# Kernel tuning notes

Hardware: AMD Instinct MI355X
Metric: run time of the kernel (lower is better)

Reference implementation:

```python
import jax, jax.numpy as jnp
import numpy as np

N = 100_000      # nodes
E = 1_600_000    # edges (avg degree 16)
D = 64           # dim_node
H = 64           # dim_hidden
L = 4            # model_layer
G = 512          # num graphs
BN_EPS = 1e-5


def setup_inputs() -> dict:
    key = jax.random.key(0)
    ks = jax.random.split(key, 16)
    x = jax.random.normal(ks[0], (N, D), dtype=jnp.float32)
    edge_index = jax.random.randint(ks[1], (2, E), 0, N, dtype=jnp.int64)
    batch = jnp.sort(jax.random.randint(ks[2], (N,), 0, G, dtype=jnp.int64))
    s = 0.05
    # stacked per-layer params (all layers same shape since D == H)
    W1 = jax.random.normal(ks[3], (L, D, 2 * H), dtype=jnp.float32) * s
    b1 = jax.random.normal(ks[4], (L, 2 * H), dtype=jnp.float32) * s
    g1 = 1.0 + jax.random.normal(ks[5], (L, 2 * H), dtype=jnp.float32) * 0.1
    bt1 = jax.random.normal(ks[6], (L, 2 * H), dtype=jnp.float32) * 0.1
    m1 = jax.random.normal(ks[7], (L, 2 * H), dtype=jnp.float32) * 0.1
    v1 = jax.random.uniform(ks[8], (L, 2 * H), dtype=jnp.float32, minval=0.5, maxval=1.5)
    W2 = jax.random.normal(ks[9], (L, 2 * H, H), dtype=jnp.float32) * s
    b2 = jax.random.normal(ks[10], (L, H), dtype=jnp.float32) * s
    g2 = 1.0 + jax.random.normal(ks[11], (L, H), dtype=jnp.float32) * 0.1
    bt2 = jax.random.normal(ks[12], (L, H), dtype=jnp.float32) * 0.1
    m2 = jax.random.normal(ks[13], (L, H), dtype=jnp.float32) * 0.1
    v2 = jax.random.uniform(ks[14], (L, H), dtype=jnp.float32, minval=0.5, maxval=1.5)
    return {"x": x, "edge_index": edge_index, "batch": batch,
            "W1": W1, "b1": b1, "g1": g1, "bt1": bt1, "m1": m1, "v1": v1,
            "W2": W2, "b2": b2, "g2": g2, "bt2": bt2, "m2": m2, "v2": v2}


def _bn(h, m, v, g, b):
    # inference-mode BatchNorm1d with running stats
    return (h - m) * jax.lax.rsqrt(v + BN_EPS) * g + b


def reference(x, edge_index, batch, W1, b1, g1, bt1, m1, v1, W2, b2, g2, bt2, m2, v2):
    src, dst = edge_index[0], edge_index[1]
    h = x
    for i in range(L):
        # GINConv with eps=0: nn(x + sum_{j in N(i)} x_j)
        agg = jax.ops.segment_sum(h[src], dst, num_segments=N)  # [N, d]
        z = h + agg
        z = z @ W1[i] + b1[i]                 # [N, 2H]
        z = jax.nn.relu(_bn(z, m1[i], v1[i], g1[i], bt1[i]))
        z = z @ W2[i] + b2[i]                 # [N, H]
        z = _bn(z, m2[i], v2[i], g2[i], bt2[i])  # outer BatchNorm
        if i != L - 1:                        # ReLU skipped on final layer
            z = jax.nn.relu(z)
        # dropout = identity in eval mode
        h = z
    # global mean pool per graph
    sums = jax.ops.segment_sum(h, batch, num_segments=G)                    # [G, H]
    cnts = jax.ops.segment_sum(jnp.ones((N, 1), h.dtype), batch, num_segments=G)
    return sums / jnp.maximum(cnts, 1.0)
```

## Files before the change

kernel.cpp:

```cpp
#include <hip/hip_runtime.h>
#include <hip/hip_bf16.h>

#define N_NODES 100000
#define N_EDGES 1600000
#define N_GRAPHS 512
#define BN_EPS 1e-5f
#define BM 128
#define NB_MLP ((N_NODES + BM - 1) / BM)
#define CB_SHIFT 9
#define NCB ((N_NODES + 511) / 512)
#define FB_EPB 4096
#define FB_BLOCKS ((N_EDGES + FB_EPB - 1) / FB_EPB)
#define SEG_CAP 11264

typedef short v8s __attribute__((ext_vector_type(8)));
typedef float v4f __attribute__((ext_vector_type(4)));

__device__ __forceinline__ unsigned short f2bf(float f) {
    union { float f; unsigned int i; } c; c.f = f;
    unsigned int lsb = (c.i >> 16) & 1;
    unsigned int r = c.i + 0x7FFFu + lsb;
    return (unsigned short)(r >> 16);
}
__device__ __forceinline__ float bflo(unsigned int u) {
    union { unsigned int i; float f; } c; c.i = u << 16; return c.f;
}
__device__ __forceinline__ float bfhi(unsigned int u) {
    union { unsigned int i; float f; } c; c.i = u & 0xFFFF0000u; return c.f;
}
__device__ __forceinline__ unsigned int packbf(float a, float b) {
    return (unsigned int)f2bf(a) | ((unsigned int)f2bf(b) << 16);
}
__device__ __forceinline__ int clampn(int v) {
    return v < 0 ? 0 : (v >= N_NODES ? N_NODES - 1 : v);
}

__global__ void convert_kernel(const float4* __restrict__ x, uint2* __restrict__ xb, int n16) {
    int i = blockIdx.x * blockDim.x + threadIdx.x;
    if (i < n16) {
        float4 a = x[i];
        uint2 u;
        u.x = packbf(a.x, a.y);
        u.y = packbf(a.z, a.w);
        xb[i] = u;
    }
}

__global__ void zero_small_kernel(int* __restrict__ p, int n) {
    int i = blockIdx.x * blockDim.x + threadIdx.x;
    if (i < n) p[i] = 0;
}

__launch_bounds__(256)
__global__ void cbhist_kernel(const int* __restrict__ ei, int* __restrict__ cbcnt) {
    __shared__ int h[NCB];
    int tid = threadIdx.x;
    for (int b = tid; b < NCB; b += 256) h[b] = 0;
    __syncthreads();
    int e0 = blockIdx.x * FB_EPB;
    int e1 = e0 + FB_EPB;
    if (e1 > N_EDGES) e1 = N_EDGES;
    for (int e = e0 + tid; e < e1; e += 256)
        atomicAdd(&h[clampn(ei[N_EDGES + e]) >> CB_SHIFT], 1);
    __syncthreads();
    for (int b = tid; b < NCB; b += 256)
        if (h[b] > 0) atomicAdd(&cbcnt[b], h[b]);
}

__global__ void cbscan_kernel(const int* __restrict__ cbcnt,
                              int* __restrict__ bucket_base, int* __restrict__ gcur) {
    __shared__ int s[NCB];
    int tid = threadIdx.x;
    for (int i = tid; i < NCB; i += 256) s[i] = cbcnt[i];
    __syncthreads();
    if (tid == 0) {
        int run = 0;
        for (int i = 0; i < NCB; ++i) { int v = s[i]; s[i] = run; run += v; }
    }
    __syncthreads();
    for (int i = tid; i < NCB; i += 256) { bucket_base[i] = s[i]; gcur[i] = s[i]; }
    if (tid == 0) bucket_base[NCB] = N_EDGES;
}

__launch_bounds__(256)
__global__ void binfill_kernel(const int* __restrict__ ei, int* __restrict__ gcur,
                               unsigned int* __restrict__ bpk) {
    __shared__ int cnt[NCB];
    __shared__ int gbase[NCB];
    __shared__ int lcur[NCB];
    int tid = threadIdx.x;
    int e0 = blockIdx.x * FB_EPB;
    int e1 = e0 + FB_EPB;
    if (e1 > N_EDGES) e1 = N_EDGES;

    for (int b = tid; b < NCB; b += 256) cnt[b] = 0;
    __syncthreads();
    for (int e = e0 + tid; e < e1; e += 256) {
        int d = clampn(ei[N_EDGES + e]);
        atomicAdd(&cnt[d >> CB_SHIFT], 1);
    }
    __syncthreads();
    for (int b = tid; b < NCB; b += 256) {
        int c = cnt[b];
        gbase[b] = (c > 0) ? atomicAdd(&gcur[b], c) : 0;
        lcur[b] = 0;
    }
    __syncthreads();
    for (int e = e0 + tid; e < e1; e += 256) {
        int s = clampn(ei[e]);
        int d = clampn(ei[N_EDGES + e]);
        int b = d >> CB_SHIFT;
        int lpos = atomicAdd(&lcur[b], 1);
        bpk[gbase[b] + lpos] = ((unsigned int)s << CB_SHIFT) | (unsigned int)(d & 511);
    }
}

__launch_bounds__(256)
__global__ void binscatter_kernel(const unsigned int* __restrict__ bpk,
                                  const int* __restrict__ bucket_base,
                                  int* __restrict__ row_start,
                                  int* __restrict__ adj) {
    __shared__ int seg[SEG_CAP];
    __shared__ int lcnt[512];
    __shared__ int lpre[512];

    int b = blockIdx.x;
    int tid = threadIdx.x;
    int nlo = b << CB_SHIFT;
    int nn = N_NODES - nlo; if (nn > 512) nn = 512;
    int base = bucket_base[b];
    int cnt  = bucket_base[b + 1] - base;

    lcnt[tid] = 0; lcnt[tid + 256] = 0;
    __syncthreads();
    for (int e = tid; e < cnt; e += 256)
        atomicAdd(&lcnt[bpk[base + e] & 511u], 1);
    __syncthreads();
    int i0 = tid, i1 = tid + 256;
    lpre[i0] = lcnt[i0]; lpre[i1] = lcnt[i1];
    __syncthreads();
    for (int st = 1; st < 512; st <<= 1) {
        int v0 = (i0 >= st) ? lpre[i0 - st] : 0;
        int v1 = (i1 >= st) ? lpre[i1 - st] : 0;
        __syncthreads();
        lpre[i0] += v0; lpre[i1] += v1;
        __syncthreads();
    }
    {
        int ex0 = lpre[i0] - lcnt[i0];
        int ex1 = lpre[i1] - lcnt[i1];
        if (i0 < nn) row_start[nlo + i0] = base + ex0;
        if (i1 < nn) row_start[nlo + i1] = base + ex1;
        lcnt[i0] = ex0;
        lcnt[i1] = ex1;
    }
    if (b == NCB - 1 && tid == 0) row_start[N_NODES] = N_EDGES;
    __syncthreads();

    if (cnt <= SEG_CAP) {
        for (int e = tid; e < cnt; e += 256) {
            unsigned int u = bpk[base + e];
            int pos = atomicAdd(&lcnt[u & 511u], 1);
            seg[pos] = (int)(u >> CB_SHIFT);
        }
        __syncthreads();
        for (int i = tid; i < cnt; i += 256) adj[base + i] = seg[i];
    } else {
        for (int e = tid; e < cnt; e += 256) {
            unsigned int u = bpk[base + e];
            int pos = atomicAdd(&lcnt[u & 511u], 1);
            adj[base + pos] = (int)(u >> CB_SHIFT);
        }
    }
}

#define GATHER_BLOCKS 2048
__global__ void gather_kernel(const unsigned short* __restrict__ hin,
                              unsigned short* __restrict__ zb,
                              const int* __restrict__ row_start,
                              const int* __restrict__ adj) {
    const unsigned int* hu = (const unsigned int*)hin;
    unsigned int* zu = (unsigned int*)zb;
    const int j2 = threadIdx.x & 31;
    const int unit = (blockIdx.x * blockDim.x + threadIdx.x) >> 5;
    const int nunits = (gridDim.x * blockDim.x) >> 5;

    for (int n = unit; n < N_NODES; n += nunits) {
        int beg = row_start[n];
        int end = row_start[n + 1];
        unsigned int us = hu[(size_t)n * 32 + j2];
        float s0 = bflo(us), s1 = bfhi(us);

        int i = beg;
        for (; i + 8 <= end; i += 8) {
            int a0 = adj[i],     a1 = adj[i + 1], a2 = adj[i + 2], a3 = adj[i + 3];
            int a4 = adj[i + 4], a5 = adj[i + 5], a6 = adj[i + 6], a7 = adj[i + 7];
            unsigned int u0 = hu[(size_t)a0 * 32 + j2];
            unsigned int u1 = hu[(size_t)a1 * 32 + j2];
            unsigned int u2 = hu[(size_t)a2 * 32 + j2];
            unsigned int u3 = hu[(size_t)a3 * 32 + j2];
            unsigned int u4 = hu[(size_t)a4 * 32 + j2];
            unsigned int u5 = hu[(size_t)a5 * 32 + j2];
            unsigned int u6 = hu[(size_t)a6 * 32 + j2];
            unsigned int u7 = hu[(size_t)a7 * 32 + j2];
            s0 += ((bflo(u0) + bflo(u1)) + (bflo(u2) + bflo(u3)))
                + ((bflo(u4) + bflo(u5)) + (bflo(u6) + bflo(u7)));
            s1 += ((bfhi(u0) + bfhi(u1)) + (bfhi(u2) + bfhi(u3)))
                + ((bfhi(u4) + bfhi(u5)) + (bfhi(u6) + bfhi(u7)));
        }
        if (i + 4 <= end) {
            int a0 = adj[i], a1 = adj[i + 1], a2 = adj[i + 2], a3 = adj[i + 3];
            unsigned int u0 = hu[(size_t)a0 * 32 + j2];
            unsigned int u1 = hu[(size_t)a1 * 32 + j2];
            unsigned int u2 = hu[(size_t)a2 * 32 + j2];
            unsigned int u3 = hu[(size_t)a3 * 32 + j2];
            s0 += (bflo(u0) + bflo(u1)) + (bflo(u2) + bflo(u3));
            s1 += (bfhi(u0) + bfhi(u1)) + (bfhi(u2) + bfhi(u3));
            i += 4;
        }
        if (i + 2 <= end) {
            int a0 = adj[i], a1 = adj[i + 1];
            unsigned int u0 = hu[(size_t)a0 * 32 + j2];
            unsigned int u1 = hu[(size_t)a1 * 32 + j2];
            s0 += bflo(u0) + bflo(u1);
            s1 += bfhi(u0) + bfhi(u1);
            i += 2;
        }
        if (i < end) {
            unsigned int u0 = hu[(size_t)adj[i] * 32 + j2];
            s0 += bflo(u0);
            s1 += bfhi(u0);
        }

        zu[(size_t)n * 32 + j2] = packbf(s0, s1);
    }
}

__launch_bounds__(256)
__global__ void mlp_mfma_kernel(const unsigned short* __restrict__ zg,
                                unsigned short* __restrict__ hb,
                                const float* __restrict__ W1, const float* __restrict__ b1,
                                const float* __restrict__ g1, const float* __restrict__ bt1,
                                const float* __restrict__ m1, const float* __restrict__ v1,
                                const float* __restrict__ W2, const float* __restrict__ b2,
                                const float* __restrict__ g2, const float* __restrict__ bt2,
                                const float* __restrict__ m2, const float* __restrict__ v2,
                                int relu_out) {
    __shared__ __align__(16) char smem[53760];
    float* s1p = (float*)(smem);
    float* o1p = (float*)(smem + 512);
    float* o2p = (float*)(smem + 1024);
    float* s2p = (float*)(smem + 1280);
    short* tb  = (short*)(smem + 1536);
    short* w1b = (short*)(smem + 1536);
    short* w2b = (short*)(smem + 36352);

    const int tid = threadIdx.x;
    const int nbase = blockIdx.x * BM;

    if (tid < 128) {
        float sv = g1[tid] * rsqrtf(v1[tid] + BN_EPS);
        s1p[tid] = sv;
        o1p[tid] = (b1[tid] - m1[tid]) * sv + bt1[tid];
    } else if (tid < 192) {
        int j = tid - 128;
        float sv = g2[j] * rsqrtf(v2[j] + BN_EPS);
        s2p[j] = sv;
        o2p[j] = (b2[j] - m2[j]) * sv + bt2[j];
    }
    __syncthreads();

    {
        int n = tid & 127;
        int kc = tid >> 7;
        float sv = s1p[n];
        for (int k = kc * 32; k < kc * 32 + 32; k += 2) {
            float w0 = W1[k * 128 + n] * sv;
            float w1 = W1[(k + 1) * 128 + n] * sv;
            unsigned int u = (unsigned int)f2bf(w0) | ((unsigned int)f2bf(w1) << 16);
            *(unsigned int*)(w1b + n * 72 + k) = u;
        }
    }
    {
        int jo = tid & 63;
        int c = tid >> 6;
        float sv = s2p[jo];
        for (int jh = c * 32; jh < c * 32 + 32; jh += 2) {
            float w0 = W2[jh * 64 + jo] * sv;
            float w1 = W2[(jh + 1) * 64 + jo] * sv;
            unsigned int u = (unsigned int)f2bf(w0) | ((unsigned int)f2bf(w1) << 16);
            *(unsigned int*)(w2b + jo * 136 + jh) = u;
        }
    }
    __syncthreads();

    const int wave = tid >> 6;
    const int lane = tid & 63;
    const int lr = lane & 15;
    const int quad = lane >> 4;
    const int m0 = wave * 32;

    int ra0 = nbase + m0 + lr;       ra0 = ra0 < N_NODES ? ra0 : N_NODES - 1;
    int ra1 = nbase + m0 + 16 + lr;  ra1 = ra1 < N_NODES ? ra1 : N_NODES - 1;
    const v8s* pa0 = (const v8s*)(zg + (size_t)ra0 * 64 + quad * 8);
    const v8s* pa1 = (const v8s*)(zg + (size_t)ra1 * 64 + quad * 8);
    v8s a0k[2], a1k[2];
    a0k[0] = pa0[0]; a0k[1] = pa0[4];
    a1k[0] = pa1[0]; a1k[1] = pa1[4];

    v4f acc1[2][8];
    #pragma unroll
    for (int rt = 0; rt < 2; ++rt)
        #pragma unroll
        for (int ct = 0; ct < 8; ++ct)
            acc1[rt][ct] = (v4f){0.f, 0.f, 0.f, 0.f};

    #pragma unroll
    for (int ks = 0; ks < 2; ++ks) {
        int kb = ks * 32 + quad * 8;
        #pragma unroll
        for (int ct = 0; ct < 8; ++ct) {
            v8s bF = *(const v8s*)(w1b + (ct * 16 + lr) * 72 + kb);
            acc1[0][ct] = __builtin_amdgcn_mfma_f32_16x16x32_bf16(a0k[ks], bF, acc1[0][ct], 0, 0, 0);
            acc1[1][ct] = __builtin_amdgcn_mfma_f32_16x16x32_bf16(a1k[ks], bF, acc1[1][ct], 0, 0, 0);
        }
    }

    __syncthreads();

    #pragma unroll
    for (int rt = 0; rt < 2; ++rt) {
        #pragma unroll
        for (int ct = 0; ct < 8; ++ct) {
            int col = ct * 16 + lr;
            float o1v = o1p[col];
            #pragma unroll
            for (int r = 0; r < 4; ++r) {
                float v = acc1[rt][ct][r] + o1v;
                v = fmaxf(v, 0.0f);
                int row = m0 + rt * 16 + quad * 4 + r;
                tb[row * 136 + col] = (short)f2bf(v);
            }
        }
    }

    v4f acc2[2][4];
    #pragma unroll
    for (int rt = 0; rt < 2; ++rt)
        #pragma unroll
        for (int ct = 0; ct < 4; ++ct)
            acc2[rt][ct] = (v4f){0.f, 0.f, 0.f, 0.f};

    #pragma unroll
    for (int ks = 0; ks < 4; ++ks) {
        int kb = ks * 32 + quad * 8;
        v8s a0 = *(const v8s*)(tb + (m0 + lr) * 136 + kb);
        v8s a1 = *(const v8s*)(tb + (m0 + 16 + lr) * 136 + kb);
        #pragma unroll
        for (int ct = 0; ct < 4; ++ct) {
            v8s bF = *(const v8s*)(w2b + (ct * 16 + lr) * 136 + kb);
            acc2[0][ct] = __builtin_amdgcn_mfma_f32_16x16x32_bf16(a0, bF, acc2[0][ct], 0, 0, 0);
            acc2[1][ct] = __builtin_amdgcn_mfma_f32_16x16x32_bf16(a1, bF, acc2[1][ct], 0, 0, 0);
        }
    }

    #pragma unroll
    for (int rt = 0; rt < 2; ++rt) {
        #pragma unroll
        for (int ct = 0; ct < 4; ++ct) {
            int col = ct * 16 + lr;
            float o2v = o2p[col];
            #pragma unroll
            for (int r = 0; r < 4; ++r) {
                int row = m0 + rt * 16 + quad * 4 + r;
                int n = nbase + row;
                if (n < N_NODES) {
                    float v = acc2[rt][ct][r] + o2v;
                    if (relu_out) v = fmaxf(v, 0.0f);
                    hb[(size_t)n * 64 + col] = f2bf(v);
                }
            }
        }
    }
}

__launch_bounds__(256)
__global__ void pool_kernel(const unsigned short* __restrict__ hb,
                            const int* __restrict__ batch,
                            float* __restrict__ out) {
    __shared__ float part[4][64];
    int g = blockIdx.x;
    int tid = threadIdx.x;
    int w = tid >> 6;
    int j = tid & 63;

    int lo = 0, hi = N_NODES;
    while (lo < hi) { int mid = (lo + hi) >> 1; if (batch[mid] < g) lo = mid + 1; else hi = mid; }
    int start = lo;
    hi = N_NODES;
    while (lo < hi) { int mid = (lo + hi) >> 1; if (batch[mid] < g + 1) lo = mid + 1; else hi = mid; }
    int end = lo;

    float sum = 0.0f;
    int n = start + w;
    for (; n + 4 < end; n += 8) {
        unsigned int ua = (unsigned int)hb[(size_t)n * 64 + j];
        unsigned int ub = (unsigned int)hb[(size_t)(n + 4) * 64 + j];
        union { unsigned int i; float f; } ca, cb;
        ca.i = ua << 16; cb.i = ub << 16;
        sum += ca.f + cb.f;
    }
    if (n < end) {
        unsigned int u = (unsigned int)hb[(size_t)n * 64 + j];
        union { unsigned int i; float f; } c; c.i = u << 16;
        sum += c.f;
    }
    part[w][j] = sum;
    __syncthreads();
    if (w == 0) {
        float s = (part[0][j] + part[1][j]) + (part[2][j] + part[3][j]);
        float cnt = (float)(end - start);
        out[g * 64 + j] = s / fmaxf(cnt, 1.0f);
    }
}

extern "C" void kernel_launch(void* const* d_in, const int* in_sizes, int n_in,
                              void* d_out, int out_size, void* d_ws, size_t ws_size,
                              hipStream_t stream) {
    const float* x   = (const float*)d_in[0];
    const int* ei    = (const int*)d_in[1];
    const int* batch = (const int*)d_in[2];
    const float* W1  = (const float*)d_in[3];
    const float* b1  = (const float*)d_in[4];
    const float* g1  = (const float*)d_in[5];
    const float* bt1 = (const float*)d_in[6];
    const float* m1  = (const float*)d_in[7];
    const float* v1  = (const float*)d_in[8];
    const float* W2  = (const float*)d_in[9];
    const float* b2  = (const float*)d_in[10];
    const float* g2  = (const float*)d_in[11];
    const float* bt2 = (const float*)d_in[12];
    const float* m2  = (const float*)d_in[13];
    const float* v2  = (const float*)d_in[14];

    unsigned short* hb = (unsigned short*)d_ws;
    unsigned short* xb = hb + (size_t)N_NODES * 64;
    unsigned short* zb = xb + (size_t)N_NODES * 64;
    int* row_start = (int*)(zb + (size_t)N_NODES * 64);
    int* adj       = row_start + N_NODES + 1;
    int* cbcnt     = adj + N_EDGES;
    int* bucket_base = cbcnt + NCB;
    int* gcur      = bucket_base + NCB + 1;
    unsigned int* bpk = (unsigned int*)(gcur + NCB);

    float* out = (float*)d_out;

    const int n16 = N_NODES * 16;
    convert_kernel<<<(n16 + 255) / 256, 256, 0, stream>>>((const float4*)x, (uint2*)xb, n16);

    zero_small_kernel<<<1, 256, 0, stream>>>(cbcnt, NCB);
    cbhist_kernel<<<FB_BLOCKS, 256, 0, stream>>>(ei, cbcnt);
    cbscan_kernel<<<1, 256, 0, stream>>>(cbcnt, bucket_base, gcur);
    binfill_kernel<<<FB_BLOCKS, 256, 0, stream>>>(ei, gcur, bpk);
    binscatter_kernel<<<NCB, 256, 0, stream>>>(bpk, bucket_base, row_start, adj);

    for (int l = 0; l < 4; ++l) {
        const unsigned short* hin = (l == 0) ? xb : hb;
        gather_kernel<<<GATHER_BLOCKS, 256, 0, stream>>>(hin, zb, row_start, adj);
        mlp_mfma_kernel<<<NB_MLP, 256, 0, stream>>>(
            zb, hb,
            W1 + (size_t)l * 64 * 128, b1 + l * 128, g1 + l * 128, bt1 + l * 128,
            m1 + l * 128, v1 + l * 128,
            W2 + (size_t)l * 128 * 64, b2 + l * 64, g2 + l * 64, bt2 + l * 64,
            m2 + l * 64, v2 + l * 64,
            (l != 3) ? 1 : 0);
    }

    pool_kernel<<<N_GRAPHS, 256, 0, stream>>>(hb, batch, out);
}
```

Baseline: 376.3 us.

## Fuse neighbor gather into per-layer MLP kernel with ping-pong feature buffers

Merges the separate gather kernel into the MFMA MLP kernel: each block of 128 nodes aggregates its neighbours into shared memory and then runs both GEMMs from there, so the intermediate z buffer is never written to or read back from global memory. Because a layer now reads h while writing the next h, two feature buffers are alternated. The zeroing of the bucket counters is also folded into the convert kernel, which removes one launch. In exchange the gather now runs on only about 782 blocks with larger shared memory, so fewer waves may be in flight to hide the random-gather latency.

After: 620.5 us. 1.65x slower.

```diff
diff --git a/kernel.cpp b/kernel.cpp
--- a/kernel.cpp
+++ b/kernel.cpp
@@ -35,8 +35,10 @@
     return v < 0 ? 0 : (v >= N_NODES ? N_NODES - 1 : v);
 }
 
-__global__ void convert_kernel(const float4* __restrict__ x, uint2* __restrict__ xb, int n16) {
+__global__ void convert_kernel(const float4* __restrict__ x, uint2* __restrict__ xb,
+                               int n16, int* __restrict__ cbcnt) {
     int i = blockIdx.x * blockDim.x + threadIdx.x;
+    if (blockIdx.x == 0 && threadIdx.x < NCB) cbcnt[threadIdx.x] = 0;
     if (i < n16) {
         float4 a = x[i];
         uint2 u;
@@ -44,11 +46,6 @@
         u.y = packbf(a.z, a.w);
         xb[i] = u;
     }
-}
-
-__global__ void zero_small_kernel(int* __restrict__ p, int n) {
-    int i = blockIdx.x * blockDim.x + threadIdx.x;
-    if (i < n) p[i] = 0;
 }
 
 __launch_bounds__(256)
@@ -174,89 +171,31 @@
     }
 }
 
-#define GATHER_BLOCKS 2048
-__global__ void gather_kernel(const unsigned short* __restrict__ hin,
-                              unsigned short* __restrict__ zb,
-                              const int* __restrict__ row_start,
-                              const int* __restrict__ adj) {
-    const unsigned int* hu = (const unsigned int*)hin;
-    unsigned int* zu = (unsigned int*)zb;
-    const int j2 = threadIdx.x & 31;
-    const int unit = (blockIdx.x * blockDim.x + threadIdx.x) >> 5;
-    const int nunits = (gridDim.x * blockDim.x) >> 5;
-
-    for (int n = unit; n < N_NODES; n += nunits) {
-        int beg = row_start[n];
-        int end = row_start[n + 1];
-        unsigned int us = hu[(size_t)n * 32 + j2];
-        float s0 = bflo(us), s1 = bfhi(us);
-
-        int i = beg;
-        for (; i + 8 <= end; i += 8) {
-            int a0 = adj[i],     a1 = adj[i + 1], a2 = adj[i + 2], a3 = adj[i + 3];
-            int a4 = adj[i + 4], a5 = adj[i + 5], a6 = adj[i + 6], a7 = adj[i + 7];
-            unsigned int u0 = hu[(size_t)a0 * 32 + j2];
-            unsigned int u1 = hu[(size_t)a1 * 32 + j2];
-            unsigned int u2 = hu[(size_t)a2 * 32 + j2];
-            unsigned int u3 = hu[(size_t)a3 * 32 + j2];
-            unsigned int u4 = hu[(size_t)a4 * 32 + j2];
-            unsigned int u5 = hu[(size_t)a5 * 32 + j2];
-            unsigned int u6 = hu[(size_t)a6 * 32 + j2];
-            unsigned int u7 = hu[(size_t)a7 * 32 + j2];
-            s0 += ((bflo(u0) + bflo(u1)) + (bflo(u2) + bflo(u3)))
-                + ((bflo(u4) + bflo(u5)) + (bflo(u6) + bflo(u7)));
-            s1 += ((bfhi(u0) + bfhi(u1)) + (bfhi(u2) + bfhi(u3)))
-                + ((bfhi(u4) + bfhi(u5)) + (bfhi(u6) + bfhi(u7)));
-        }
-        if (i + 4 <= end) {
-            int a0 = adj[i], a1 = adj[i + 1], a2 = adj[i + 2], a3 = adj[i + 3];
-            unsigned int u0 = hu[(size_t)a0 * 32 + j2];
-            unsigned int u1 = hu[(size_t)a1 * 32 + j2];
-            unsigned int u2 = hu[(size_t)a2 * 32 + j2];
-            unsigned int u3 = hu[(size_t)a3 * 32 + j2];
-            s0 += (bflo(u0) + bflo(u1)) + (bflo(u2) + bflo(u3));
-            s1 += (bfhi(u0) + bfhi(u1)) + (bfhi(u2) + bfhi(u3));
-            i += 4;
-        }
-        if (i + 2 <= end) {
-            int a0 = adj[i], a1 = adj[i + 1];
-            unsigned int u0 = hu[(size_t)a0 * 32 + j2];
-            unsigned int u1 = hu[(size_t)a1 * 32 + j2];
-            s0 += bflo(u0) + bflo(u1);
-            s1 += bfhi(u0) + bfhi(u1);
-            i += 2;
-        }
-        if (i < end) {
-            unsigned int u0 = hu[(size_t)adj[i] * 32 + j2];
-            s0 += bflo(u0);
-            s1 += bfhi(u0);
-        }
-
-        zu[(size_t)n * 32 + j2] = packbf(s0, s1);
-    }
-}
-
 __launch_bounds__(256)
-__global__ void mlp_mfma_kernel(const unsigned short* __restrict__ zg,
-                                unsigned short* __restrict__ hb,
-                                const float* __restrict__ W1, const float* __restrict__ b1,
-                                const float* __restrict__ g1, const float* __restrict__ bt1,
-                                const float* __restrict__ m1, const float* __restrict__ v1,
-                                const float* __restrict__ W2, const float* __restrict__ b2,
-                                const float* __restrict__ g2, const float* __restrict__ bt2,
-                                const float* __restrict__ m2, const float* __restrict__ v2,
-                                int relu_out) {
-    __shared__ __align__(16) char smem[53760];
-    float* s1p = (float*)(smem);
-    float* o1p = (float*)(smem + 512);
-    float* o2p = (float*)(smem + 1024);
-    float* s2p = (float*)(smem + 1280);
-    short* tb  = (short*)(smem + 1536);
-    short* w1b = (short*)(smem + 1536);
-    short* w2b = (short*)(smem + 36352);
+__global__ void layer_kernel(const unsigned short* __restrict__ hin,
+                             unsigned short* __restrict__ hout,
+                             const int* __restrict__ row_start,
+                             const int* __restrict__ adj,
+                             const float* __restrict__ W1, const float* __restrict__ b1,
+                             const float* __restrict__ g1, const float* __restrict__ bt1,
+                             const float* __restrict__ m1, const float* __restrict__ v1,
+                             const float* __restrict__ W2, const float* __restrict__ b2,
+                             const float* __restrict__ g2, const float* __restrict__ bt2,
+                             const float* __restrict__ m2, const float* __restrict__ v2,
+                             int relu_out) {
+    __shared__ __align__(16) char smem[55808];
+    short* zbl = (short*)(smem);
+    short* w1b = (short*)(smem + 18432);
+    short* tb  = (short*)(smem);
+    short* w2b = (short*)(smem + 36864);
+    float* s1p = (float*)(smem + 54272);
+    float* o1p = (float*)(smem + 54784);
+    float* s2p = (float*)(smem + 55296);
+    float* o2p = (float*)(smem + 55552);
 
     const int tid = threadIdx.x;
     const int nbase = blockIdx.x * BM;
+    const unsigned int* hu = (const unsigned int*)hin;
 
     if (tid < 128) {
         float sv = g1[tid] * rsqrtf(v1[tid] + BN_EPS);
@@ -292,6 +231,61 @@
             *(unsigned int*)(w2b + jo * 136 + jh) = u;
         }
     }
+
+    {
+        const int hw = tid >> 5;
+        const int j2 = tid & 31;
+        for (int r = hw; r < BM; r += 8) {
+            int n = nbase + r;
+            n = n < N_NODES ? n : N_NODES - 1;
+            int beg = row_start[n];
+            int end = row_start[n + 1];
+            unsigned int us = hu[(size_t)n * 32 + j2];
+            float s0 = bflo(us), s1 = bfhi(us);
+
+            int i = beg;
+            for (; i + 8 <= end; i += 8) {
+                int a0 = adj[i],     a1 = adj[i + 1], a2 = adj[i + 2], a3 = adj[i + 3];
+                int a4 = adj[i + 4], a5 = adj[i + 5], a6 = adj[i + 6], a7 = adj[i + 7];
+                unsigned int u0 = hu[(size_t)a0 * 32 + j2];
+                unsigned int u1 = hu[(size_t)a1 * 32 + j2];
+                unsigned int u2 = hu[(size_t)a2 * 32 + j2];
+                unsigned int u3 = hu[(size_t)a3 * 32 + j2];
+                unsigned int u4 = hu[(size_t)a4 * 32 + j2];
+                unsigned int u5 = hu[(size_t)a5 * 32 + j2];
+                unsigned int u6 = hu[(size_t)a6 * 32 + j2];
+                unsigned int u7 = hu[(size_t)a7 * 32 + j2];
+                s0 += ((bflo(u0) + bflo(u1)) + (bflo(u2) + bflo(u3)))
+                    + ((bflo(u4) + bflo(u5)) + (bflo(u6) + bflo(u7)));
+                s1 += ((bfhi(u0) + bfhi(u1)) + (bfhi(u2) + bfhi(u3)))
+                    + ((bfhi(u4) + bfhi(u5)) + (bfhi(u6) + bfhi(u7)));
+            }
+            if (i + 4 <= end) {
+                int a0 = adj[i], a1 = adj[i + 1], a2 = adj[i + 2], a3 = adj[i + 3];
+                unsigned int u0 = hu[(size_t)a0 * 32 + j2];
+                unsigned int u1 = hu[(size_t)a1 * 32 + j2];
+                unsigned int u2 = hu[(size_t)a2 * 32 + j2];
+                unsigned int u3 = hu[(size_t)a3 * 32 + j2];
+                s0 += (bflo(u0) + bflo(u1)) + (bflo(u2) + bflo(u3));
+                s1 += (bfhi(u0) + bfhi(u1)) + (bfhi(u2) + bfhi(u3));
+                i += 4;
+            }
+            if (i + 2 <= end) {
+                int a0 = adj[i], a1 = adj[i + 1];
+                unsigned int u0 = hu[(size_t)a0 * 32 + j2];
+                unsigned int u1 = hu[(size_t)a1 * 32 + j2];
+                s0 += bflo(u0) + bflo(u1);
+                s1 += bfhi(u0) + bfhi(u1);
+                i += 2;
+            }
+            if (i < end) {
+                unsigned int u0 = hu[(size_t)adj[i] * 32 + j2];
+                s0 += bflo(u0);
+                s1 += bfhi(u0);
+            }
+            *(unsigned int*)(zbl + r * 72 + j2 * 2) = packbf(s0, s1);
+        }
+    }
     __syncthreads();
 
     const int wave = tid >> 6;
@@ -300,13 +294,12 @@
     const int quad = lane >> 4;
     const int m0 = wave * 32;
 
-    int ra0 = nbase + m0 + lr;       ra0 = ra0 < N_NODES ? ra0 : N_NODES - 1;
-    int ra1 = nbase + m0 + 16 + lr;  ra1 = ra1 < N_NODES ? ra1 : N_NODES - 1;
-    const v8s* pa0 = (const v8s*)(zg + (size_t)ra0 * 64 + quad * 8);
-    const v8s* pa1 = (const v8s*)(zg + (size_t)ra1 * 64 + quad * 8);
     v8s a0k[2], a1k[2];
-    a0k[0] = pa0[0]; a0k[1] = pa0[4];
-    a1k[0] = pa1[0]; a1k[1] = pa1[4];
+    #pragma unroll
+    for (int ks = 0; ks < 2; ++ks) {
+        a0k[ks] = *(const v8s*)(zbl + (m0 + lr) * 72 + ks * 32 + quad * 8);
+        a1k[ks] = *(const v8s*)(zbl + (m0 + 16 + lr) * 72 + ks * 32 + quad * 8);
+    }
 
     v4f acc1[2][8];
     #pragma unroll
@@ -377,7 +370,7 @@
                 if (n < N_NODES) {
                     float v = acc2[rt][ct][r] + o2v;
                     if (relu_out) v = fmaxf(v, 0.0f);
-                    hb[(size_t)n * 64 + col] = f2bf(v);
+                    hout[(size_t)n * 64 + col] = f2bf(v);
                 }
             }
         }
@@ -443,10 +436,10 @@
     const float* m2  = (const float*)d_in[13];
     const float* v2  = (const float*)d_in[14];
 
-    unsigned short* hb = (unsigned short*)d_ws;
-    unsigned short* xb = hb + (size_t)N_NODES * 64;
-    unsigned short* zb = xb + (size_t)N_NODES * 64;
-    int* row_start = (int*)(zb + (size_t)N_NODES * 64);
+    unsigned short* h0 = (unsigned short*)d_ws;
+    unsigned short* h1 = h0 + (size_t)N_NODES * 64;
+    unsigned short* xb = h1 + (size_t)N_NODES * 64;
+    int* row_start = (int*)(xb + (size_t)N_NODES * 64);
     int* adj       = row_start + N_NODES + 1;
     int* cbcnt     = adj + N_EDGES;
     int* bucket_base = cbcnt + NCB;
@@ -456,25 +449,26 @@
     float* out = (float*)d_out;
 
     const int n16 = N_NODES * 16;
-    convert_kernel<<<(n16 + 255) / 256, 256, 0, stream>>>((const float4*)x, (uint2*)xb, n16);
-
-    zero_small_kernel<<<1, 256, 0, stream>>>(cbcnt, NCB);
+    convert_kernel<<<(n16 + 255) / 256, 256, 0, stream>>>(
+        (const float4*)x, (uint2*)xb, n16, cbcnt);
     cbhist_kernel<<<FB_BLOCKS, 256, 0, stream>>>(ei, cbcnt);
     cbscan_kernel<<<1, 256, 0, stream>>>(cbcnt, bucket_base, gcur);
     binfill_kernel<<<FB_BLOCKS, 256, 0, stream>>>(ei, gcur, bpk);
     binscatter_kernel<<<NCB, 256, 0, stream>>>(bpk, bucket_base, row_start, adj);
 
+    const unsigned short* hin = xb;
+    unsigned short* hout = h0;
     for (int l = 0; l < 4; ++l) {
-        const unsigned short* hin = (l == 0) ? xb : hb;
-        gather_kernel<<<GATHER_BLOCKS, 256, 0, stream>>>(hin, zb, row_start, adj);
-        mlp_mfma_kernel<<<NB_MLP, 256, 0, stream>>>(
-            zb, hb,
+        layer_kernel<<<NB_MLP, 256, 0, stream>>>(
+            hin, hout, row_start, adj,
             W1 + (size_t)l * 64 * 128, b1 + l * 128, g1 + l * 128, bt1 + l * 128,
             m1 + l * 128, v1 + l * 128,
             W2 + (size_t)l * 128 * 64, b2 + l * 64, g2 + l * 64, bt2 + l * 64,
             m2 + l * 64, v2 + l * 64,
             (l != 3) ? 1 : 0);
-    }
-
-    pool_kernel<<<N_GRAPHS, 256, 0, stream>>>(hb, batch, out);
-}
+        hin = hout;
+        hout = (hout == h0) ? h1 : h0;
+    }
+
+    pool_kernel<<<N_GRAPHS, 256, 0, stream>>>(h1, batch, out);
+}
```
